# Kernel optimization log

Measured on AMD Instinct MI355X. Metric: run time of the kernel, lower is better.

## Reference

```python
import jax, jax.numpy as jnp
import numpy as np

INPUT_SIZE = 4
HIDDEN = 50
OUTPUT = 1


def setup_inputs() -> dict:
    key = jax.random.key(0)
    ks = jax.random.split(key, 7)
    B, T = 4096, 512
    scale_ih = 1.0 / np.sqrt(HIDDEN)
    seq = jax.random.normal(ks[0], (B, T, INPUT_SIZE), dtype=jnp.float32)
    # PyTorch LSTM params, gate order (i, f, g, o) stacked along first dim
    W_ih = jax.random.uniform(ks[1], (4 * HIDDEN, INPUT_SIZE), jnp.float32, -scale_ih, scale_ih)
    W_hh = jax.random.uniform(ks[2], (4 * HIDDEN, HIDDEN), jnp.float32, -scale_ih, scale_ih)
    b_ih = jax.random.uniform(ks[3], (4 * HIDDEN,), jnp.float32, -scale_ih, scale_ih)
    b_hh = jax.random.uniform(ks[4], (4 * HIDDEN,), jnp.float32, -scale_ih, scale_ih)
    W_out = jax.random.uniform(ks[5], (OUTPUT, HIDDEN), jnp.float32, -scale_ih, scale_ih)
    b_out = jax.random.uniform(ks[6], (OUTPUT,), jnp.float32, -scale_ih, scale_ih)
    return {"seq": seq, "W_ih": W_ih, "W_hh": W_hh, "b_ih": b_ih, "b_hh": b_hh,
            "W_out": W_out, "b_out": b_out}


def _lstm_last_hidden(seq, W_ih, W_hh, b_ih, b_hh):
    B = seq.shape[0]
    H = HIDDEN
    # precompute input contribution for all timesteps: [T, B, 4H]
    x_gates = jnp.einsum('bti,gi->tbg', seq, W_ih) + (b_ih + b_hh)

    def step(carry, xg):
        h, c = carry
        gates = xg + h @ W_hh.T  # [B, 4H]
        i = jax.nn.sigmoid(gates[:, 0*H:1*H])
        f = jax.nn.sigmoid(gates[:, 1*H:2*H])
        g = jnp.tanh(gates[:, 2*H:3*H])
        o = jax.nn.sigmoid(gates[:, 3*H:4*H])
        c = f * c + i * g
        h = o * jnp.tanh(c)
        return (h, c), None

    h0 = jnp.zeros((B, H), dtype=seq.dtype)
    c0 = jnp.zeros((B, H), dtype=seq.dtype)
    (h_last, _), _ = jax.lax.scan(step, (h0, c0), x_gates)
    return h_last


def reference(seq, W_ih, W_hh, b_ih, b_hh, W_out, b_out):
    h_last = _lstm_last_hidden(seq, W_ih, W_hh, b_ih, b_hh)  # [B, H]
    return h_last @ W_out.T + b_out  # [B, 1]
```

## Files before the change

### kernel.cpp

```cpp
#include <hip/hip_runtime.h>

typedef __attribute__((ext_vector_type(8))) short bf16x8;
typedef __attribute__((ext_vector_type(4))) float f32x4;

#define HID 50
#define TSTEPS 512
#define LOG2E 1.4426950408889634f

static __device__ __forceinline__ short f2bf(float f) {
    unsigned u = __builtin_bit_cast(unsigned, f);
    u = (u + 0x7fffu + ((u >> 16) & 1u)) >> 16;
    return (short)u;
}

static __device__ __forceinline__ float fexp2(float x) {
#if __has_builtin(__builtin_amdgcn_exp2f)
    return __builtin_amdgcn_exp2f(x);
#else
    return exp2f(x);
#endif
}
static __device__ __forceinline__ float frcp(float x) {
#if __has_builtin(__builtin_amdgcn_rcpf)
    return __builtin_amdgcn_rcpf(x);
#else
    return 1.0f / x;
#endif
}
static __device__ __forceinline__ float sigm(float x) {
    return frcp(1.0f + fexp2(-LOG2E * x));
}
static __device__ __forceinline__ float tanh_(float x) {
    return 1.0f - 2.0f * frcp(1.0f + fexp2(2.0f * LOG2E * x));
}

static __device__ __forceinline__ void lds_barrier() {
    asm volatile("s_waitcnt lgkmcnt(0)" ::: "memory");
    __builtin_amdgcn_sched_barrier(0);
    __builtin_amdgcn_s_barrier();
}

__global__ __launch_bounds__(256) void lstm_fused(
    const float* __restrict__ seq,
    const float* __restrict__ W_ih,
    const float* __restrict__ W_hh,
    const float* __restrict__ b_ih,
    const float* __restrict__ b_hh,
    const float* __restrict__ W_out,
    const float* __restrict__ b_out,
    float* __restrict__ out)
{
    __shared__ __align__(16) short h_lds[2 * 16 * 64];
    __shared__ float h32[16][51];

    const int tid = threadIdx.x;
    const int l   = tid & 63;
    const int wv  = tid >> 6;
    const int l15 = l & 15;
    const int lq  = l >> 4;
    const int jl  = wv * 16 + l15;
    const bool jv = (jl < HID);
    const int rowbase = blockIdx.x << 4;
    const int swz = (l15 & 7) << 4;

    for (int i = tid; i < 2 * 16 * 64; i += 256) h_lds[i] = 0;

    bf16x8 Bf[4][2];
#pragma unroll
    for (int g = 0; g < 4; ++g)
#pragma unroll
        for (int kk = 0; kk < 2; ++kk) {
            bf16x8 v;
#pragma unroll
            for (int e = 0; e < 8; ++e) {
                int k = kk * 32 + lq * 8 + e;
                float val = 0.0f;
                if (jv) {
                    if (k < HID)            val = W_hh[(g * HID + jl) * HID + k];
                    else if (k < HID + 4)   val = W_ih[(g * HID + jl) * 4 + (k - HID)];
                    else if (k == HID + 4)  val = b_ih[g * HID + jl] + b_hh[g * HID + jl];
                }
                v[e] = f2bf(val);
            }
            Bf[g][kk] = v;
        }

    const char* xp = (const char*)seq + (size_t)(rowbase + l15) * TSTEPS * 16;
    float4 sqA = make_float4(0.f, 0.f, 0.f, 0.f);
    float4 sqB = make_float4(0.f, 0.f, 0.f, 0.f);
    if (lq == 2) {
        sqA = *(const float4*)(xp);
        sqB = *(const float4*)(xp + 16);
    }

    float c[4] = {0.f, 0.f, 0.f, 0.f};
    float h[4] = {0.f, 0.f, 0.f, 0.f};

    const char* rdA = (const char*)h_lds + l15 * 128 + ((lq * 16) ^ swz);
    const char* rdB = (const char*)h_lds + l15 * 128 + ((64 + lq * 16) ^ swz);
    char* wb[4];
#pragma unroll
    for (int r = 0; r < 4; ++r) {
        int row = lq * 4 + r;
        wb[r] = (char*)h_lds + row * 128 + ((2 * jl) ^ ((row & 7) << 4));
    }

    __syncthreads();

#define STEP(TT, SQ, RDOFF, WROFF)                                                             \
    {                                                                                          \
        bf16x8 a0 = *(const bf16x8*)(rdA + (RDOFF));                                           \
        bf16x8 a1 = *(const bf16x8*)(rdB + (RDOFF));                                           \
        if (lq == 2) {                                                                         \
            a1[2] = f2bf(SQ.x); a1[3] = f2bf(SQ.y);                                            \
            a1[4] = f2bf(SQ.z); a1[5] = f2bf(SQ.w);                                            \
            a1[6] = (short)0x3f80;                                        \
        }                                                                                      \
        if ((TT) + 2 < TSTEPS && lq == 2)                                                      \
            SQ = *(const float4*)(xp + ((TT) + 2) * 16);  \
        f32x4 ac0 = {0.f,0.f,0.f,0.f}, ac1 = {0.f,0.f,0.f,0.f};                                \
        f32x4 ac2 = {0.f,0.f,0.f,0.f}, ac3 = {0.f,0.f,0.f,0.f};                                \
        ac0 = __builtin_amdgcn_mfma_f32_16x16x32_bf16(a0, Bf[0][0], ac0, 0, 0, 0);             \
        ac1 = __builtin_amdgcn_mfma_f32_16x16x32_bf16(a0, Bf[1][0], ac1, 0, 0, 0);             \
        ac2 = __builtin_amdgcn_mfma_f32_16x16x32_bf16(a0, Bf[2][0], ac2, 0, 0, 0);             \
        ac3 = __builtin_amdgcn_mfma_f32_16x16x32_bf16(a0, Bf[3][0], ac3, 0, 0, 0);             \
        ac0 = __builtin_amdgcn_mfma_f32_16x16x32_bf16(a1, Bf[0][1], ac0, 0, 0, 0);             \
        ac1 = __builtin_amdgcn_mfma_f32_16x16x32_bf16(a1, Bf[1][1], ac1, 0, 0, 0);             \
        ac2 = __builtin_amdgcn_mfma_f32_16x16x32_bf16(a1, Bf[2][1], ac2, 0, 0, 0);             \
        ac3 = __builtin_amdgcn_mfma_f32_16x16x32_bf16(a1, Bf[3][1], ac3, 0, 0, 0);             \
        _Pragma("unroll")                                                                      \
        for (int r = 0; r < 4; ++r) {                                                          \
            float iv = sigm(ac0[r]), fv = sigm(ac1[r]);                                        \
            float gv = tanh_(ac2[r]), ov = sigm(ac3[r]);                                       \
            c[r] = fv * c[r] + iv * gv;                                                        \
            h[r] = ov * tanh_(c[r]);                                                           \
        }                                                                                      \
        if (jv) {                                                                              \
            _Pragma("unroll")                                                                  \
            for (int r = 0; r < 4; ++r)                                                        \
                *(short*)(wb[r] + (WROFF)) = f2bf(h[r]);                                       \
        }                                                                                      \
        lds_barrier();                                                                         \
    }

    for (int t = 0; t < TSTEPS; t += 2) {
        STEP(t,     sqA, 0,    2048);
        STEP(t + 1, sqB, 2048, 0);
    }
#undef STEP

    if (jv) {
#pragma unroll
        for (int r = 0; r < 4; ++r) h32[lq * 4 + r][jl] = h[r];
    }
    __syncthreads();
    if (tid < 16) {
        float s = b_out[0];
        for (int j = 0; j < HID; ++j) s += h32[tid][j] * W_out[j];
        out[rowbase + tid] = s;
    }
}

extern "C" void kernel_launch(void* const* d_in, const int* in_sizes, int n_in,
                              void* d_out, int out_size, void* d_ws, size_t ws_size,
                              hipStream_t stream) {
    const float* seq   = (const float*)d_in[0];
    const float* W_ih  = (const float*)d_in[1];
    const float* W_hh  = (const float*)d_in[2];
    const float* b_ih  = (const float*)d_in[3];
    const float* b_hh  = (const float*)d_in[4];
    const float* W_out = (const float*)d_in[5];
    const float* b_out = (const float*)d_in[6];
    float* out = (float*)d_out;

    const int B = in_sizes[0] / (TSTEPS * 4);
    lstm_fused<<<dim3(B / 16), dim3(256), 0, stream>>>(
        seq, W_ih, W_hh, b_ih, b_hh, W_out, b_out, out);
}
```

Baseline: 347.0 us.

## Split batch rows into two interleaved groups to overlap MFMA with gate activations

Splits each wave's four accumulator rows into two groups, A and B, and software-pipelines them. In each phase one group's gate activations and cell update run while the MFMAs for the other group's next step are issued. The h buffer grows from double to quadruple buffering to support the interleave. The aim is to hide MFMA latency behind the transcendental work on the serial recurrence chain. In exchange, every phase issues the full set of 16x16 MFMAs while using only half the output rows, and there are twice as many LDS barriers per timestep.

```diff
diff --git a/kernel.cpp b/kernel.cpp
--- a/kernel.cpp
+++ b/kernel.cpp
@@ -50,7 +50,7 @@
     const float* __restrict__ b_out,
     float* __restrict__ out)
 {
-    __shared__ __align__(16) short h_lds[2 * 16 * 64];
+    __shared__ __align__(16) short h_lds[4 * 16 * 64];
     __shared__ float h32[16][51];
 
     const int tid = threadIdx.x;
@@ -63,7 +63,7 @@
     const int rowbase = blockIdx.x << 4;
     const int swz = (l15 & 7) << 4;
 
-    for (int i = tid; i < 2 * 16 * 64; i += 256) h_lds[i] = 0;
+    for (int i = tid; i < 4 * 16 * 64; i += 256) h_lds[i] = 0;
 
     bf16x8 Bf[4][2];
 #pragma unroll
@@ -86,72 +86,134 @@
         }
 
     const char* xp = (const char*)seq + (size_t)(rowbase + l15) * TSTEPS * 16;
-    float4 sqA = make_float4(0.f, 0.f, 0.f, 0.f);
-    float4 sqB = make_float4(0.f, 0.f, 0.f, 0.f);
+    float4 xE = make_float4(0.f, 0.f, 0.f, 0.f);
+    float4 xO = make_float4(0.f, 0.f, 0.f, 0.f);
     if (lq == 2) {
-        sqA = *(const float4*)(xp);
-        sqB = *(const float4*)(xp + 16);
-    }
-
-    float c[4] = {0.f, 0.f, 0.f, 0.f};
-    float h[4] = {0.f, 0.f, 0.f, 0.f};
-
-    const char* rdA = (const char*)h_lds + l15 * 128 + ((lq * 16) ^ swz);
-    const char* rdB = (const char*)h_lds + l15 * 128 + ((64 + lq * 16) ^ swz);
-    char* wb[4];
-#pragma unroll
-    for (int r = 0; r < 4; ++r) {
-        int row = lq * 4 + r;
-        wb[r] = (char*)h_lds + row * 128 + ((2 * jl) ^ ((row & 7) << 4));
-    }
+        xE = *(const float4*)(xp);
+        xO = *(const float4*)(xp + 16);
+    }
+
+    float cA0 = 0.f, cA1 = 0.f, hA0 = 0.f, hA1 = 0.f;
+    float cB0 = 0.f, cB1 = 0.f, hB0 = 0.f, hB1 = 0.f;
+
+    const char* rd0 = (const char*)h_lds + l15 * 128 + ((lq * 16) ^ swz);
+    const char* rd1 = (const char*)h_lds + l15 * 128 + ((64 + lq * 16) ^ swz);
+    const int rA0 = lq * 4, rA1 = rA0 + 1, rB0 = rA0 + 2, rB1 = rA0 + 3;
+    char* wbA0 = (char*)h_lds + rA0 * 128 + ((2 * jl) ^ ((rA0 & 7) << 4));
+    char* wbA1 = (char*)h_lds + rA1 * 128 + ((2 * jl) ^ ((rA1 & 7) << 4));
+    char* wbB0 = (char*)h_lds + rB0 * 128 + ((2 * jl) ^ ((rB0 & 7) << 4));
+    char* wbB1 = (char*)h_lds + rB1 * 128 + ((2 * jl) ^ ((rB1 & 7) << 4));
 
     __syncthreads();
 
-#define STEP(TT, SQ, RDOFF, WROFF)                                                             \
+    f32x4 aA0 = {0.f,0.f,0.f,0.f}, aA1 = {0.f,0.f,0.f,0.f};
+    f32x4 aA2 = {0.f,0.f,0.f,0.f}, aA3 = {0.f,0.f,0.f,0.f};
+    f32x4 aB0 = {0.f,0.f,0.f,0.f}, aB1 = {0.f,0.f,0.f,0.f};
+    f32x4 aB2 = {0.f,0.f,0.f,0.f}, aB3 = {0.f,0.f,0.f,0.f};
+    {
+        bf16x8 a0 = {0,0,0,0,0,0,0,0};
+        bf16x8 a1 = {0,0,0,0,0,0,0,0};
+        if (lq == 2) {
+            a1[2] = f2bf(xE.x); a1[3] = f2bf(xE.y);
+            a1[4] = f2bf(xE.z); a1[5] = f2bf(xE.w);
+            a1[6] = (short)0x3f80;
+        }
+        aA0 = __builtin_amdgcn_mfma_f32_16x16x32_bf16(a0, Bf[0][0], aA0, 0, 0, 0);
+        aA1 = __builtin_amdgcn_mfma_f32_16x16x32_bf16(a0, Bf[1][0], aA1, 0, 0, 0);
+        aA2 = __builtin_amdgcn_mfma_f32_16x16x32_bf16(a0, Bf[2][0], aA2, 0, 0, 0);
+        aA3 = __builtin_amdgcn_mfma_f32_16x16x32_bf16(a0, Bf[3][0], aA3, 0, 0, 0);
+        aA0 = __builtin_amdgcn_mfma_f32_16x16x32_bf16(a1, Bf[0][1], aA0, 0, 0, 0);
+        aA1 = __builtin_amdgcn_mfma_f32_16x16x32_bf16(a1, Bf[1][1], aA1, 0, 0, 0);
+        aA2 = __builtin_amdgcn_mfma_f32_16x16x32_bf16(a1, Bf[2][1], aA2, 0, 0, 0);
+        aA3 = __builtin_amdgcn_mfma_f32_16x16x32_bf16(a1, Bf[3][1], aA3, 0, 0, 0);
+    }
+
+#define PHASE_A(TA_WR, TB_RD, XREG)                                                            \
     {                                                                                          \
-        bf16x8 a0 = *(const bf16x8*)(rdA + (RDOFF));                                           \
-        bf16x8 a1 = *(const bf16x8*)(rdB + (RDOFF));                                           \
+        bf16x8 a0 = *(const bf16x8*)(rd0 + (TB_RD));                                           \
+        bf16x8 a1 = *(const bf16x8*)(rd1 + (TB_RD));                                           \
         if (lq == 2) {                                                                         \
-            a1[2] = f2bf(SQ.x); a1[3] = f2bf(SQ.y);                                            \
-            a1[4] = f2bf(SQ.z); a1[5] = f2bf(SQ.w);                                            \
-            a1[6] = (short)0x3f80;                                        \
-        }                                                                                      \
-        if ((TT) + 2 < TSTEPS && lq == 2)                                                      \
-            SQ = *(const float4*)(xp + ((TT) + 2) * 16);  \
-        f32x4 ac0 = {0.f,0.f,0.f,0.f}, ac1 = {0.f,0.f,0.f,0.f};                                \
-        f32x4 ac2 = {0.f,0.f,0.f,0.f}, ac3 = {0.f,0.f,0.f,0.f};                                \
-        ac0 = __builtin_amdgcn_mfma_f32_16x16x32_bf16(a0, Bf[0][0], ac0, 0, 0, 0);             \
-        ac1 = __builtin_amdgcn_mfma_f32_16x16x32_bf16(a0, Bf[1][0], ac1, 0, 0, 0);             \
-        ac2 = __builtin_amdgcn_mfma_f32_16x16x32_bf16(a0, Bf[2][0], ac2, 0, 0, 0);             \
-        ac3 = __builtin_amdgcn_mfma_f32_16x16x32_bf16(a0, Bf[3][0], ac3, 0, 0, 0);             \
-        ac0 = __builtin_amdgcn_mfma_f32_16x16x32_bf16(a1, Bf[0][1], ac0, 0, 0, 0);             \
-        ac1 = __builtin_amdgcn_mfma_f32_16x16x32_bf16(a1, Bf[1][1], ac1, 0, 0, 0);             \
-        ac2 = __builtin_amdgcn_mfma_f32_16x16x32_bf16(a1, Bf[2][1], ac2, 0, 0, 0);             \
-        ac3 = __builtin_amdgcn_mfma_f32_16x16x32_bf16(a1, Bf[3][1], ac3, 0, 0, 0);             \
-        _Pragma("unroll")                                                                      \
-        for (int r = 0; r < 4; ++r) {                                                          \
-            float iv = sigm(ac0[r]), fv = sigm(ac1[r]);                                        \
-            float gv = tanh_(ac2[r]), ov = sigm(ac3[r]);                                       \
-            c[r] = fv * c[r] + iv * gv;                                                        \
-            h[r] = ov * tanh_(c[r]);                                                           \
+            a1[2] = f2bf(XREG.x); a1[3] = f2bf(XREG.y);                                        \
+            a1[4] = f2bf(XREG.z); a1[5] = f2bf(XREG.w);                                        \
+            a1[6] = (short)0x3f80;                                                             \
+        }                                                                                      \
+        {                                                                                      \
+            float iv = sigm(aA0[0]), fv = sigm(aA1[0]), gv = tanh_(aA2[0]), ov = sigm(aA3[0]); \
+            cA0 = fv * cA0 + iv * gv;  hA0 = ov * tanh_(cA0);                                  \
+        }                                                                                      \
+        {                                                                                      \
+            float iv = sigm(aA0[1]), fv = sigm(aA1[1]), gv = tanh_(aA2[1]), ov = sigm(aA3[1]); \
+            cA1 = fv * cA1 + iv * gv;  hA1 = ov * tanh_(cA1);                                  \
         }                                                                                      \
         if (jv) {                                                                              \
-            _Pragma("unroll")                                                                  \
-            for (int r = 0; r < 4; ++r)                                                        \
-                *(short*)(wb[r] + (WROFF)) = f2bf(h[r]);                                       \
-        }                                                                                      \
+            *(short*)(wbA0 + (TA_WR)) = f2bf(hA0);                                             \
+            *(short*)(wbA1 + (TA_WR)) = f2bf(hA1);                                             \
+        }                                                                                      \
+        aB0 = (f32x4){0.f,0.f,0.f,0.f}; aB1 = (f32x4){0.f,0.f,0.f,0.f};                        \
+        aB2 = (f32x4){0.f,0.f,0.f,0.f}; aB3 = (f32x4){0.f,0.f,0.f,0.f};                        \
+        aB0 = __builtin_amdgcn_mfma_f32_16x16x32_bf16(a0, Bf[0][0], aB0, 0, 0, 0);             \
+        aB1 = __builtin_amdgcn_mfma_f32_16x16x32_bf16(a0, Bf[1][0], aB1, 0, 0, 0);             \
+        aB2 = __builtin_amdgcn_mfma_f32_16x16x32_bf16(a0, Bf[2][0], aB2, 0, 0, 0);             \
+        aB3 = __builtin_amdgcn_mfma_f32_16x16x32_bf16(a0, Bf[3][0], aB3, 0, 0, 0);             \
+        aB0 = __builtin_amdgcn_mfma_f32_16x16x32_bf16(a1, Bf[0][1], aB0, 0, 0, 0);             \
+        aB1 = __builtin_amdgcn_mfma_f32_16x16x32_bf16(a1, Bf[1][1], aB1, 0, 0, 0);             \
+        aB2 = __builtin_amdgcn_mfma_f32_16x16x32_bf16(a1, Bf[2][1], aB2, 0, 0, 0);             \
+        aB3 = __builtin_amdgcn_mfma_f32_16x16x32_bf16(a1, Bf[3][1], aB3, 0, 0, 0);             \
         lds_barrier();                                                                         \
     }
 
+#define PHASE_B(TB_WR, TA_RD, XREG)                                                            \
+    {                                                                                          \
+        bf16x8 a0 = *(const bf16x8*)(rd0 + (TA_RD));                                           \
+        bf16x8 a1 = *(const bf16x8*)(rd1 + (TA_RD));                                           \
+        if (lq == 2) {                                                                         \
+            a1[2] = f2bf(XREG.x); a1[3] = f2bf(XREG.y);                                        \
+            a1[4] = f2bf(XREG.z); a1[5] = f2bf(XREG.w);                                        \
+            a1[6] = (short)0x3f80;                                                             \
+        }                                                                                      \
+        {                                                                                      \
+            float iv = sigm(aB0[2]), fv = sigm(aB1[2]), gv = tanh_(aB2[2]), ov = sigm(aB3[2]); \
+            cB0 = fv * cB0 + iv * gv;  hB0 = ov * tanh_(cB0);                                  \
+        }                                                                                      \
+        {                                                                                      \
+            float iv = sigm(aB0[3]), fv = sigm(aB1[3]), gv = tanh_(aB2[3]), ov = sigm(aB3[3]); \
+            cB1 = fv * cB1 + iv * gv;  hB1 = ov * tanh_(cB1);                                  \
+        }                                                                                      \
+        if (jv) {                                                                              \
+            *(short*)(wbB0 + (TB_WR)) = f2bf(hB0);                                             \
+            *(short*)(wbB1 + (TB_WR)) = f2bf(hB1);                                             \
+        }                                                                                      \
+        aA0 = (f32x4){0.f,0.f,0.f,0.f}; aA1 = (f32x4){0.f,0.f,0.f,0.f};                        \
+        aA2 = (f32x4){0.f,0.f,0.f,0.f}; aA3 = (f32x4){0.f,0.f,0.f,0.f};                        \
+        aA0 = __builtin_amdgcn_mfma_f32_16x16x32_bf16(a0, Bf[0][0], aA0, 0, 0, 0);             \
+        aA1 = __builtin_amdgcn_mfma_f32_16x16x32_bf16(a0, Bf[1][0], aA1, 0, 0, 0);             \
+        aA2 = __builtin_amdgcn_mfma_f32_16x16x32_bf16(a0, Bf[2][0], aA2, 0, 0, 0);             \
+        aA3 = __builtin_amdgcn_mfma_f32_16x16x32_bf16(a0, Bf[3][0], aA3, 0, 0, 0);             \
+        aA0 = __builtin_amdgcn_mfma_f32_16x16x32_bf16(a1, Bf[0][1], aA0, 0, 0, 0);             \
+        aA1 = __builtin_amdgcn_mfma_f32_16x16x32_bf16(a1, Bf[1][1], aA1, 0, 0, 0);             \
+        aA2 = __builtin_amdgcn_mfma_f32_16x16x32_bf16(a1, Bf[2][1], aA2, 0, 0, 0);             \
+        aA3 = __builtin_amdgcn_mfma_f32_16x16x32_bf16(a1, Bf[3][1], aA3, 0, 0, 0);             \
+        lds_barrier();                                                                         \
+    }
+
     for (int t = 0; t < TSTEPS; t += 2) {
-        STEP(t,     sqA, 0,    2048);
-        STEP(t + 1, sqB, 2048, 0);
-    }
-#undef STEP
+        PHASE_A(2048, 4096, xE);
+        if (t + 2 < TSTEPS && lq == 2)
+            xE = *(const float4*)(xp + (t + 2) * 16);
+        PHASE_B(6144, 2048, xO);
+        PHASE_A(0, 6144, xO);
+        if (t + 3 < TSTEPS && lq == 2)
+            xO = *(const float4*)(xp + (t + 3) * 16);
+        PHASE_B(4096, 0, xE);
+    }
+#undef PHASE_A
+#undef PHASE_B
 
     if (jv) {
-#pragma unroll
-        for (int r = 0; r < 4; ++r) h32[lq * 4 + r][jl] = h[r];
+        h32[rA0][jl] = hA0;
+        h32[rA1][jl] = hA1;
+        h32[rB0][jl] = hB0;
+        h32[rB1][jl] = hB1;
     }
     __syncthreads();
     if (tid < 16) {
```

Result: slower. 473.9 us (+36.6%).

## Halve batch rows per block and redistribute gate nonlinearities across all lanes via LDS

Applied to the files above, without the earlier changes.

Each block now handles 8 batch rows instead of 16, doubling the number of blocks to spread the latency-bound recurrence across more CUs. The MFMA still runs 16 rows with 8 as padding; lanes holding the valid rows write their gate pre-activations to an LDS scratch buffer, and every lane then reads back two (row, hidden) pairs. This splits the transcendental work evenly instead of repeating it four times per lane, and h is written as packed bf16 pairs. It adds an LDS round trip per timestep and wastes half of the MFMA work.

```diff
diff --git a/kernel.cpp b/kernel.cpp
--- a/kernel.cpp
+++ b/kernel.cpp
@@ -51,7 +51,8 @@
     float* __restrict__ out)
 {
     __shared__ __align__(16) short h_lds[2 * 16 * 64];
-    __shared__ float h32[16][51];
+    __shared__ __align__(16) float scr[4 * 512];
+    __shared__ float h32[8][51];
 
     const int tid = threadIdx.x;
     const int l   = tid & 63;
@@ -60,7 +61,7 @@
     const int lq  = l >> 4;
     const int jl  = wv * 16 + l15;
     const bool jv = (jl < HID);
-    const int rowbase = blockIdx.x << 4;
+    const int rowbase = blockIdx.x << 3;
     const int swz = (l15 & 7) << 4;
 
     for (int i = tid; i < 2 * 16 * 64; i += 256) h_lds[i] = 0;
@@ -86,38 +87,45 @@
         }
 
     const char* xp = (const char*)seq + (size_t)(rowbase + l15) * TSTEPS * 16;
-    float4 sqA = make_float4(0.f, 0.f, 0.f, 0.f);
-    float4 sqB = make_float4(0.f, 0.f, 0.f, 0.f);
-    if (lq == 2) {
-        sqA = *(const float4*)(xp);
-        sqB = *(const float4*)(xp + 16);
-    }
-
-    float c[4] = {0.f, 0.f, 0.f, 0.f};
-    float h[4] = {0.f, 0.f, 0.f, 0.f};
+    const bool xl = (lq == 2) && (l15 < 8);
+    float4 xE = make_float4(0.f, 0.f, 0.f, 0.f);
+    float4 xO = make_float4(0.f, 0.f, 0.f, 0.f);
+    if (xl) {
+        xE = *(const float4*)(xp);
+        xO = *(const float4*)(xp + 16);
+    }
 
     const char* rdA = (const char*)h_lds + l15 * 128 + ((lq * 16) ^ swz);
     const char* rdB = (const char*)h_lds + l15 * 128 + ((64 + lq * 16) ^ swz);
-    char* wb[4];
-#pragma unroll
-    for (int r = 0; r < 4; ++r) {
-        int row = lq * 4 + r;
-        wb[r] = (char*)h_lds + row * 128 + ((2 * jl) ^ ((row & 7) << 4));
-    }
+
+    char* const swb = (char*)(scr + wv * 512);
+    char* const pw0 = swb + lq * 1024 + ((l15 ^ (lq << 1)) << 4);
+    char* const pw1 = swb + lq * 1024 + 256 + ((l15 ^ 1 ^ (lq << 1)) << 4);
+
+    const int arow = l >> 3;
+    const int jj0  = (l & 7) << 1;
+    const bool rodd = (arow & 1) != 0;
+    const char* const pr = swb + arow * 256 + ((jj0 ^ ((arow >> 2) << 1)) << 4);
+    const int jE = wv * 16 + jj0 + (rodd ? 1 : 0);
+    const int jO = wv * 16 + jj0 + (rodd ? 0 : 1);
+    char* const hw = (char*)h_lds + arow * 128 + (((wv * 16 + jj0) * 2) ^ ((arow & 7) << 4));
+    const bool hok = (wv * 16 + jj0) <= 48;
+
+    float cE = 0.f, cO = 0.f, hE = 0.f, hO = 0.f;
 
     __syncthreads();
 
-#define STEP(TT, SQ, RDOFF, WROFF)                                                             \
+#define STEP(TT, XREG, RDOFF, WROFF)                                                           \
     {                                                                                          \
         bf16x8 a0 = *(const bf16x8*)(rdA + (RDOFF));                                           \
         bf16x8 a1 = *(const bf16x8*)(rdB + (RDOFF));                                           \
         if (lq == 2) {                                                                         \
-            a1[2] = f2bf(SQ.x); a1[3] = f2bf(SQ.y);                                            \
-            a1[4] = f2bf(SQ.z); a1[5] = f2bf(SQ.w);                                            \
+            a1[2] = f2bf(XREG.x); a1[3] = f2bf(XREG.y);                                        \
+            a1[4] = f2bf(XREG.z); a1[5] = f2bf(XREG.w);                                        \
             a1[6] = (short)0x3f80;                                        \
         }                                                                                      \
-        if ((TT) + 2 < TSTEPS && lq == 2)                                                      \
-            SQ = *(const float4*)(xp + ((TT) + 2) * 16);  \
+        if ((TT) + 2 < TSTEPS && xl)                                                           \
+            XREG = *(const float4*)(xp + ((TT) + 2) * 16);                                     \
         f32x4 ac0 = {0.f,0.f,0.f,0.f}, ac1 = {0.f,0.f,0.f,0.f};                                \
         f32x4 ac2 = {0.f,0.f,0.f,0.f}, ac3 = {0.f,0.f,0.f,0.f};                                \
         ac0 = __builtin_amdgcn_mfma_f32_16x16x32_bf16(a0, Bf[0][0], ac0, 0, 0, 0);             \
@@ -128,33 +136,46 @@
         ac1 = __builtin_amdgcn_mfma_f32_16x16x32_bf16(a1, Bf[1][1], ac1, 0, 0, 0);             \
         ac2 = __builtin_amdgcn_mfma_f32_16x16x32_bf16(a1, Bf[2][1], ac2, 0, 0, 0);             \
         ac3 = __builtin_amdgcn_mfma_f32_16x16x32_bf16(a1, Bf[3][1], ac3, 0, 0, 0);             \
-        _Pragma("unroll")                                                                      \
-        for (int r = 0; r < 4; ++r) {                                                          \
-            float iv = sigm(ac0[r]), fv = sigm(ac1[r]);                                        \
-            float gv = tanh_(ac2[r]), ov = sigm(ac3[r]);                                       \
-            c[r] = fv * c[r] + iv * gv;                                                        \
-            h[r] = ov * tanh_(c[r]);                                                           \
-        }                                                                                      \
-        if (jv) {                                                                              \
-            _Pragma("unroll")                                                                  \
-            for (int r = 0; r < 4; ++r)                                                        \
-                *(short*)(wb[r] + (WROFF)) = f2bf(h[r]);                                       \
+        if (lq < 2) {                                                                          \
+            f32x4 t0 = {ac0[0], ac1[0], ac2[0], ac3[0]};                                       \
+            f32x4 t1 = {ac0[1], ac1[1], ac2[1], ac3[1]};                                       \
+            f32x4 t2 = {ac0[2], ac1[2], ac2[2], ac3[2]};                                       \
+            f32x4 t3 = {ac0[3], ac1[3], ac2[3], ac3[3]};                                       \
+            *(f32x4*)(pw0)       = t0;                                                         \
+            *(f32x4*)(pw1)       = t1;                                                         \
+            *(f32x4*)(pw0 + 512) = t2;                                                         \
+            *(f32x4*)(pw1 + 512) = t3;                                                         \
+        }                                                                                      \
+        f32x4 qE = *(const f32x4*)(pr);               \
+        f32x4 qO = *(const f32x4*)(pr + 16);                                                   \
+        {                                                                                      \
+            float iv = sigm(qE[0]), fv = sigm(qE[1]), gv = tanh_(qE[2]), ov = sigm(qE[3]);     \
+            cE = fv * cE + iv * gv;  hE = ov * tanh_(cE);                                      \
+        }                                                                                      \
+        {                                                                                      \
+            float iv = sigm(qO[0]), fv = sigm(qO[1]), gv = tanh_(qO[2]), ov = sigm(qO[3]);     \
+            cO = fv * cO + iv * gv;  hO = ov * tanh_(cO);                                      \
+        }                                                                                      \
+        if (hok) {                                                                             \
+            unsigned uE = (unsigned short)f2bf(hE);                                            \
+            unsigned uO = (unsigned short)f2bf(hO);                                            \
+            unsigned lo = rodd ? uO : uE;                                                      \
+            unsigned hi = rodd ? uE : uO;                                                      \
+            *(unsigned*)(hw + (WROFF)) = (hi << 16) | lo;                                      \
         }                                                                                      \
         lds_barrier();                                                                         \
     }
 
     for (int t = 0; t < TSTEPS; t += 2) {
-        STEP(t,     sqA, 0,    2048);
-        STEP(t + 1, sqB, 2048, 0);
+        STEP(t,     xE, 0,    2048);
+        STEP(t + 1, xO, 2048, 0);
     }
 #undef STEP
 
-    if (jv) {
-#pragma unroll
-        for (int r = 0; r < 4; ++r) h32[lq * 4 + r][jl] = h[r];
-    }
+    if (jE < HID) h32[arow][jE] = hE;
+    if (jO < HID) h32[arow][jO] = hO;
     __syncthreads();
-    if (tid < 16) {
+    if (tid < 8) {
         float s = b_out[0];
         for (int j = 0; j < HID; ++j) s += h32[tid][j] * W_out[j];
         out[rowbase + tid] = s;
@@ -174,6 +195,6 @@
     float* out = (float*)d_out;
 
     const int B = in_sizes[0] / (TSTEPS * 4);
-    lstm_fused<<<dim3(B / 16), dim3(256), 0, stream>>>(
+    lstm_fused<<<dim3(B / 8), dim3(256), 0, stream>>>(
         seq, W_ih, W_hh, b_ih, b_hh, W_out, b_out, out);
 }
```

Measured after the change: 427.4 us. 23.2% more time.
